# Kernel optimization log

Measured on AMD Instinct MI355X. Metric: run time of the kernel, lower is better.

## Reference

```python
import jax, jax.numpy as jnp
import numpy as np

C1 = 512  # channels1 (query input dim)
C = 512   # channels (model dim)


def setup_inputs() -> dict:
    key = jax.random.key(0)
    ks = jax.random.split(key, 12)
    B, Lq, Lk = 8, 2048, 2048
    s1 = 1.0 / np.sqrt(C1)
    s = 1.0 / np.sqrt(C)
    return {
        "rep": jax.random.normal(ks[0], (B, Lq, C1), dtype=jnp.float32),
        "rep1": jax.random.normal(ks[1], (B, Lk, C), dtype=jnp.float32),
        "Wq_w": jax.random.uniform(ks[2], (C1, C), jnp.float32, -s1, s1),
        "Wq_b": jax.random.uniform(ks[3], (C,), jnp.float32, -s1, s1),
        "Wk_w": jax.random.uniform(ks[4], (C, C), jnp.float32, -s, s),
        "Wk_b": jax.random.uniform(ks[5], (C,), jnp.float32, -s, s),
        "Wv_w": jax.random.uniform(ks[6], (C, C), jnp.float32, -s, s),
        "Wv_b": jax.random.uniform(ks[7], (C,), jnp.float32, -s, s),
        "FC_w": jax.random.uniform(ks[8], (C, C), jnp.float32, -s, s),
        "FC_b": jax.random.uniform(ks[9], (C,), jnp.float32, -s, s),
    }


def reference(rep, rep1, Wq_w, Wq_b, Wk_w, Wk_b, Wv_w, Wv_b, FC_w, FC_b):
    # Linear + ReLU projections (single head)
    q = jax.nn.relu(jnp.einsum('blc,cd->bld', rep, Wq_w) + Wq_b)    # [B,Lq,C]
    k = jax.nn.relu(jnp.einsum('blc,cd->bld', rep1, Wk_w) + Wk_b)   # [B,Lk,C]
    v = jax.nn.relu(jnp.einsum('blc,cd->bld', rep1, Wv_w) + Wv_b)   # [B,Lk,C]
    scores = jnp.einsum('bqd,bkd->bqk', q, k) / jnp.sqrt(jnp.float32(C))
    attn = jax.nn.softmax(scores, axis=-1)                           # [B,Lq,Lk]
    out = jnp.einsum('bqk,bkd->bqd', attn, v)                        # [B,Lq,C]
    out = jax.nn.relu(jnp.einsum('bld,de->ble', out, FC_w) + FC_b)
    return out
```

## Files before the change

### kernel.cpp

```cpp
#include <hip/hip_runtime.h>


typedef __attribute__((ext_vector_type(8))) short short8;
typedef __attribute__((ext_vector_type(4))) float f32x4;

#define SEQ 2048
#define CH 512
#define NB 8
#define MTOT (NB * SEQ)

#define GLDS16(gp, lp)                                                                  \
  __builtin_amdgcn_global_load_lds((const __attribute__((address_space(1))) void*)(gp), \
                                   (__attribute__((address_space(3))) void*)(lp), 16, 0, 0)

__device__ __forceinline__ unsigned short f2bf(float f) {
  unsigned u = __float_as_uint(f);
  u += 0x7fffu + ((u >> 16) & 1u);
  return (unsigned short)(u >> 16);
}

__global__ void cvt_bf16_kernel(const float* __restrict__ in0, unsigned short* __restrict__ out0,
                                const float* __restrict__ in1, unsigned short* __restrict__ out1) {
  int blk = blockIdx.x;
  const float* in = (blk < 4096) ? in0 : in1;
  unsigned short* out = (blk < 4096) ? out0 : out1;
  blk &= 4095;
  long i = ((long)blk * 256 + threadIdx.x) * 8;
  float4 a = *(const float4*)(in + i);
  float4 b = *(const float4*)(in + i + 4);
  ushort4 o0, o1;
  o0.x = f2bf(a.x); o0.y = f2bf(a.y); o0.z = f2bf(a.z); o0.w = f2bf(a.w);
  o1.x = f2bf(b.x); o1.y = f2bf(b.y); o1.z = f2bf(b.z); o1.w = f2bf(b.w);
  *(ushort4*)(out + i) = o0;
  *(ushort4*)(out + i + 4) = o1;
}

__global__ __launch_bounds__(256) void wtrans_kernel(const float* __restrict__ W0,
                                                     const float* __restrict__ W1,
                                                     const float* __restrict__ W2,
                                                     const float* __restrict__ W3,
                                                     unsigned short* __restrict__ Wt) {
  __shared__ __attribute__((aligned(16))) unsigned short tile[64 * 72];
  const int z = blockIdx.z;
  const float* W = (z == 0) ? W0 : (z == 1) ? W1 : (z == 2) ? W2 : W3;
  unsigned short* Wtz = Wt + (long)z * 512 * 512;
  const int t = threadIdx.x;
  const int k0 = blockIdx.y * 64, n0 = blockIdx.x * 64;
  const int r = t >> 4, cq = (t & 15) * 4;
#pragma unroll
  for (int j = 0; j < 4; ++j) {
    int row = r + 16 * j;
    float4 v = *(const float4*)&W[(long)(k0 + row) * 512 + n0 + cq];
    tile[row * 72 + cq + 0] = f2bf(v.x);
    tile[row * 72 + cq + 1] = f2bf(v.y);
    tile[row * 72 + cq + 2] = f2bf(v.z);
    tile[row * 72 + cq + 3] = f2bf(v.w);
  }
  __syncthreads();
#pragma unroll
  for (int j = 0; j < 4; ++j) {
    int row = r + 16 * j;
    ushort4 o;
    o.x = tile[(cq + 0) * 72 + row];
    o.y = tile[(cq + 1) * 72 + row];
    o.z = tile[(cq + 2) * 72 + row];
    o.w = tile[(cq + 3) * 72 + row];
    *(ushort4*)&Wtz[(long)(n0 + row) * 512 + k0 + cq] = o;
  }
}

__global__ __launch_bounds__(256) void vtrans_kernel(const unsigned short* __restrict__ V,
                                                     unsigned short* __restrict__ Vt) {
  __shared__ __attribute__((aligned(16))) unsigned short tile[64 * 72];
  const int t = threadIdx.x;
  const int b = blockIdx.z;
  const int kk0 = blockIdx.y * 64;
  const int d0 = blockIdx.x * 64;
  const unsigned short* Vb = V + (long)b * SEQ * CH;
  unsigned short* Vtb = Vt + (long)b * CH * SEQ;
  const int r = t >> 4, cq = (t & 15) * 4;
#pragma unroll
  for (int j = 0; j < 4; ++j) {
    int row = r + 16 * j;
    ushort4 v = *(const ushort4*)&Vb[(long)(kk0 + row) * CH + d0 + cq];
    tile[row * 72 + cq + 0] = v.x;
    tile[row * 72 + cq + 1] = v.y;
    tile[row * 72 + cq + 2] = v.z;
    tile[row * 72 + cq + 3] = v.w;
  }
  __syncthreads();
#pragma unroll
  for (int j = 0; j < 4; ++j) {
    int row = r + 16 * j;
    ushort4 o;
    o.x = tile[(cq + 0) * 72 + row];
    o.y = tile[(cq + 1) * 72 + row];
    o.z = tile[(cq + 2) * 72 + row];
    o.w = tile[(cq + 3) * 72 + row];
    *(ushort4*)&Vtb[(long)(d0 + row) * SEQ + kk0 + cq] = o;
  }
}

template <int EPI, int LDA, int LDB, int LDO, int K, int BK>
__global__ __launch_bounds__(256) void gemm_nt(const unsigned short* __restrict__ A, long sAb,
                                               const unsigned short* __restrict__ Bt, long sBb,
                                               const float* __restrict__ bias,
                                               float* __restrict__ rowsum, long sRb,
                                               void* __restrict__ outp, long sOb) {
  __shared__ __attribute__((aligned(16))) unsigned short smem[2 * 128 * BK];
  unsigned short* Al = smem;
  unsigned short* Bl = smem + 128 * BK;
  const int t = threadIdx.x;
  const int w = t >> 6, l = t & 63;
  const int wr = w >> 1, wc = w & 1;
  const int lr = l & 15, lg = l >> 4;
  const int bz = blockIdx.z;
  const long m0 = (long)blockIdx.y * 128, n0 = (long)blockIdx.x * 128;
  const int NC = BK / 8;
  const int rl = l / NC, cc0 = l % NC;
  unsigned short* la = &Al[32 * w * BK];
  unsigned short* lb = &Bl[32 * w * BK];
  const unsigned short* gaJ[(BK == 128) ? 4 : 1];
  const unsigned short* gbJ[(BK == 128) ? 4 : 1];
  if (BK == 64) {
    const int srow = 32 * w + rl;
    const int sxor = (cc0 ^ (rl & 7)) * 8;
    gaJ[0] = A + bz * sAb + (long)(m0 + srow) * LDA + sxor;
    gbJ[0] = Bt + bz * sBb + (long)(n0 + srow) * LDB + sxor;
  } else {
#pragma unroll
    for (int jm = 0; jm < 4; ++jm) {
      const int srow = 32 * w + 4 * jm + rl;
      const int sxor = (cc0 ^ ((4 * jm + rl) & 15)) * 8;
      gaJ[jm] = A + bz * sAb + (long)(m0 + srow) * LDA + sxor;
      gbJ[jm] = Bt + bz * sBb + (long)(n0 + srow) * LDB + sxor;
    }
  }

  f32x4 acc[4][4] = {};
  for (int k0 = 0; k0 < K; k0 += BK) {
    if (BK == 64) {
#pragma unroll
      for (int j = 0; j < 4; ++j) {
        GLDS16(gaJ[0] + (long)8 * j * LDA, la + j * 8 * 64);
        GLDS16(gbJ[0] + (long)8 * j * LDB, lb + j * 8 * 64);
      }
      gaJ[0] += BK; gbJ[0] += BK;
    } else {
#pragma unroll
      for (int jm = 0; jm < 4; ++jm) {
        GLDS16(gaJ[jm], la + jm * 4 * 128);
        GLDS16(gaJ[jm] + (long)16 * LDA, la + (16 + 4 * jm) * 128);
        GLDS16(gbJ[jm], lb + jm * 4 * 128);
        GLDS16(gbJ[jm] + (long)16 * LDB, lb + (16 + 4 * jm) * 128);
        gaJ[jm] += BK; gbJ[jm] += BK;
      }
    }
    __syncthreads();
#pragma unroll
    for (int h = 0; h < BK / 32; ++h) {
      short8 af[4], bfr[4];
#pragma unroll
      for (int i = 0; i < 4; ++i) {
        const int kc = ((h * 4 + lg) ^ (lr & (NC - 1))) * 8;
        af[i]  = *(short8*)&Al[(64 * wr + 16 * i + lr) * BK + kc];
        bfr[i] = *(short8*)&Bl[(64 * wc + 16 * i + lr) * BK + kc];
      }
#pragma unroll
      for (int mi = 0; mi < 4; ++mi)
#pragma unroll
        for (int ni = 0; ni < 4; ++ni)
          acc[mi][ni] =
              __builtin_amdgcn_mfma_f32_16x16x32_bf16(af[mi], bfr[ni], acc[mi][ni], 0, 0, 0);
    }
    __syncthreads();
  }

  if (EPI == 1 || EPI == 6 || EPI == 2) {
    unsigned short* patch = smem;
    float bv[4];
    if (EPI == 1) {
#pragma unroll
      for (int ni = 0; ni < 4; ++ni) bv[ni] = bias[n0 + 64 * wc + 16 * ni + lr];
    }
    float rsum[4][4] = {};
#pragma unroll
    for (int mi = 0; mi < 4; ++mi)
#pragma unroll
      for (int ni = 0; ni < 4; ++ni)
#pragma unroll
        for (int r = 0; r < 4; ++r) {
          const int m = 64 * wr + 16 * mi + 4 * lg + r;
          const int n = 64 * wc + 16 * ni + lr;
          float a = acc[mi][ni][r];
          unsigned short ob;
          if (EPI == 1)      ob = f2bf(fmaxf(a + bv[ni], 0.0f));
          else if (EPI == 6) ob = f2bf(a);
          else {
            float p = exp2f(a * 0.06375872f);
            ob = f2bf(p);
            rsum[mi][r] += __uint_as_float((unsigned)ob << 16);
          }
          patch[m * 128 + ((n >> 3) ^ (m & 15)) * 8 + (n & 7)] = ob;
        }
    __syncthreads();
    unsigned short* O = (unsigned short*)outp + bz * sOb;
    const int q = t & 3;
#pragma unroll
    for (int p = 0; p < 2; ++p) {
      const int m = 64 * p + (t >> 2);
#pragma unroll
      for (int i = 0; i < 4; ++i) {
        const int cc = i * 4 + q;
        short8 x = *(short8*)&patch[m * 128 + ((cc ^ (m & 15)) * 8)];
        *(short8*)&O[(m0 + m) * LDO + n0 + cc * 8] = x;
      }
    }
    if (EPI == 2) {
      float* rsw = rowsum + bz * sRb;
#pragma unroll
      for (int off = 1; off < 16; off <<= 1)
#pragma unroll
        for (int mi = 0; mi < 4; ++mi)
#pragma unroll
          for (int r = 0; r < 4; ++r) rsum[mi][r] += __shfl_xor(rsum[mi][r], off);
      if (lr == 0) {
#pragma unroll
        for (int mi = 0; mi < 4; ++mi)
#pragma unroll
          for (int r = 0; r < 4; ++r)
            atomicAdd(&rsw[m0 + 64 * wr + 16 * mi + 4 * lg + r], rsum[mi][r]);
      }
    }
  } else {
    float* patchF = (float*)smem;
    float bv[4];
#pragma unroll
    for (int ni = 0; ni < 4; ++ni) bv[ni] = bias[n0 + 64 * wc + 16 * ni + lr];
    const float* rs = rowsum + bz * sRb;
    float inv[4][4];
#pragma unroll
    for (int mi = 0; mi < 4; ++mi)
#pragma unroll
      for (int r = 0; r < 4; ++r)
        inv[mi][r] = 1.0f / rs[m0 + 64 * wr + 16 * mi + 4 * lg + r];
#pragma unroll
    for (int mi = 0; mi < 4; ++mi)
#pragma unroll
      for (int ni = 0; ni < 4; ++ni)
#pragma unroll
        for (int r = 0; r < 4; ++r) {
          const int m = 64 * wr + 16 * mi + 4 * lg + r;
          const int n = 64 * wc + 16 * ni + lr;
          patchF[m * 128 + ((n >> 2) ^ (m & 31)) * 4 + (n & 3)] =
              fmaxf(acc[mi][ni][r] * inv[mi][r] + bv[ni], 0.0f);
        }
    __syncthreads();
    float* O = (float*)outp + bz * sOb;
    const int q = t & 3;
#pragma unroll
    for (int p = 0; p < 2; ++p) {
      const int m = 64 * p + (t >> 2);
#pragma unroll
      for (int i = 0; i < 8; ++i) {
        const int cc = i * 4 + q;
        f32x4 x = *(f32x4*)&patchF[m * 128 + ((cc ^ (m & 31)) * 4)];
        *(f32x4*)&O[(m0 + m) * LDO + n0 + cc * 4] = x;
      }
    }
  }
}

extern "C" void kernel_launch(void* const* d_in, const int* in_sizes, int n_in,
                              void* d_out, int out_size, void* d_ws, size_t ws_size,
                              hipStream_t stream) {
  const float* rep  = (const float*)d_in[0];
  const float* rep1 = (const float*)d_in[1];
  const float* Wq_w = (const float*)d_in[2];
  const float* Wq_b = (const float*)d_in[3];
  const float* Wk_w = (const float*)d_in[4];
  const float* Wk_b = (const float*)d_in[5];
  const float* Wv_w = (const float*)d_in[6];
  const float* Wv_b = (const float*)d_in[7];
  const float* FC_w = (const float*)d_in[8];
  const float* FC_b = (const float*)d_in[9];
  float* out = (float*)d_out;
  char* ws = (char*)d_ws;

  const size_t MB = 1024 * 1024;
  unsigned short* Qb     = (unsigned short*)(ws + 0 * MB);
  unsigned short* KVb    = (unsigned short*)(ws + 16 * MB);
  unsigned short* repb   = (unsigned short*)(ws + 48 * MB);
  unsigned short* rep1b  = (unsigned short*)(ws + 64 * MB);
  unsigned short* Wt4    = (unsigned short*)(ws + 80 * MB);
  float*          biasKV = (float*)(ws + 82 * MB);
  unsigned short* Pbuf   = (unsigned short*)(ws + 83 * MB);
  float*          rowsum = (float*)(ws + 147 * MB);
  const size_t need = 148 * MB;
  if (ws_size < need) return;

  unsigned short* WtQ = Wt4;
  unsigned short* WtKV = Wt4 + 512 * 512;
  unsigned short* WtF = Wt4 + 3 * 512 * 512;
  unsigned short* VFn = repb;
  unsigned short* VFt = rep1b;

  hipMemsetAsync(rowsum, 0, MTOT * 4, stream);
  hipMemcpyAsync(biasKV, Wk_b, 512 * 4, hipMemcpyDeviceToDevice, stream);
  hipMemcpyAsync(biasKV + 512, Wv_b, 512 * 4, hipMemcpyDeviceToDevice, stream);

  cvt_bf16_kernel<<<8192, 256, 0, stream>>>(rep, repb, rep1, rep1b);
  wtrans_kernel<<<dim3(8, 8, 4), 256, 0, stream>>>(Wq_w, Wk_w, Wv_w, FC_w, Wt4);

  gemm_nt<1, CH, CH, CH, CH, 64><<<dim3(4, 128, 1), 256, 0, stream>>>(
      repb, 0, WtQ, 0, Wq_b, nullptr, 0, Qb, 0);
  gemm_nt<1, CH, CH, 1024, CH, 64><<<dim3(8, 128, 1), 256, 0, stream>>>(
      rep1b, 0, WtKV, 0, biasKV, nullptr, 0, KVb, 0);

  gemm_nt<6, 1024, CH, CH, CH, 64><<<dim3(4, 16, 8), 256, 0, stream>>>(
      KVb + 512, (long)SEQ * 1024, WtF, 0, nullptr, nullptr, 0, VFn, (long)SEQ * CH);

  vtrans_kernel<<<dim3(8, 32, 8), 256, 0, stream>>>(VFn, VFt);

  gemm_nt<2, CH, 1024, SEQ, CH, 64><<<dim3(16, 16, 8), 256, 0, stream>>>(
      Qb, (long)SEQ * CH, KVb, (long)SEQ * 1024, nullptr, rowsum, SEQ,
      Pbuf, (long)SEQ * SEQ);

  gemm_nt<5, SEQ, SEQ, CH, SEQ, 128><<<dim3(4, 16, 8), 256, 0, stream>>>(
      Pbuf, (long)SEQ * SEQ, VFt, (long)CH * SEQ, FC_b, rowsum, SEQ,
      (void*)out, (long)SEQ * CH);
}
```

Before: 326.2 us.

## Merge prep and projection kernels, emit transposed VF directly, drop vtrans

Folds the bf16 conversion, weight transposes, bias copy and rowsum zeroing into one prep kernel, replacing the memset/memcpy calls. Merges the Q and KV projection GEMMs into one launch. Computes the V·FC product transposed by swapping operands, so the separate V transpose kernel goes away. Switches the final P·VF GEMM from BK=128 to BK=64. The aim is fewer launches and less transpose traffic, at the cost of less K-depth per stage in the largest GEMM.

```diff
diff --git a/kernel.cpp b/kernel.cpp
--- a/kernel.cpp
+++ b/kernel.cpp
@@ -19,143 +19,98 @@
   return (unsigned short)(u >> 16);
 }
 
-__global__ void cvt_bf16_kernel(const float* __restrict__ in0, unsigned short* __restrict__ out0,
-                                const float* __restrict__ in1, unsigned short* __restrict__ out1) {
-  int blk = blockIdx.x;
-  const float* in = (blk < 4096) ? in0 : in1;
-  unsigned short* out = (blk < 4096) ? out0 : out1;
-  blk &= 4095;
-  long i = ((long)blk * 256 + threadIdx.x) * 8;
-  float4 a = *(const float4*)(in + i);
-  float4 b = *(const float4*)(in + i + 4);
-  ushort4 o0, o1;
-  o0.x = f2bf(a.x); o0.y = f2bf(a.y); o0.z = f2bf(a.z); o0.w = f2bf(a.w);
-  o1.x = f2bf(b.x); o1.y = f2bf(b.y); o1.z = f2bf(b.z); o1.w = f2bf(b.w);
-  *(ushort4*)(out + i) = o0;
-  *(ushort4*)(out + i + 4) = o1;
-}
-
-__global__ __launch_bounds__(256) void wtrans_kernel(const float* __restrict__ W0,
-                                                     const float* __restrict__ W1,
-                                                     const float* __restrict__ W2,
-                                                     const float* __restrict__ W3,
-                                                     unsigned short* __restrict__ Wt) {
+__global__ __launch_bounds__(256) void prep_kernel(
+    const float* __restrict__ rep, const float* __restrict__ rep1,
+    unsigned short* __restrict__ repb, unsigned short* __restrict__ rep1b,
+    const float* __restrict__ W0, const float* __restrict__ W1,
+    const float* __restrict__ W2, const float* __restrict__ W3,
+    unsigned short* __restrict__ Wt,
+    const float* __restrict__ Wk_b, const float* __restrict__ Wv_b,
+    float* __restrict__ biasKV, float* __restrict__ rowsum) {
   __shared__ __attribute__((aligned(16))) unsigned short tile[64 * 72];
-  const int z = blockIdx.z;
-  const float* W = (z == 0) ? W0 : (z == 1) ? W1 : (z == 2) ? W2 : W3;
-  unsigned short* Wtz = Wt + (long)z * 512 * 512;
+  const int blk = blockIdx.x;
   const int t = threadIdx.x;
-  const int k0 = blockIdx.y * 64, n0 = blockIdx.x * 64;
-  const int r = t >> 4, cq = (t & 15) * 4;
-#pragma unroll
-  for (int j = 0; j < 4; ++j) {
-    int row = r + 16 * j;
-    float4 v = *(const float4*)&W[(long)(k0 + row) * 512 + n0 + cq];
-    tile[row * 72 + cq + 0] = f2bf(v.x);
-    tile[row * 72 + cq + 1] = f2bf(v.y);
-    tile[row * 72 + cq + 2] = f2bf(v.z);
-    tile[row * 72 + cq + 3] = f2bf(v.w);
+  if (blk < 8192) {
+    const float* in = (blk < 4096) ? rep : rep1;
+    unsigned short* out = (blk < 4096) ? repb : rep1b;
+    long i = ((long)(blk & 4095) * 256 + t) * 8;
+    float4 a = *(const float4*)(in + i);
+    float4 b = *(const float4*)(in + i + 4);
+    ushort4 o0, o1;
+    o0.x = f2bf(a.x); o0.y = f2bf(a.y); o0.z = f2bf(a.z); o0.w = f2bf(a.w);
+    o1.x = f2bf(b.x); o1.y = f2bf(b.y); o1.z = f2bf(b.z); o1.w = f2bf(b.w);
+    *(ushort4*)(out + i) = o0;
+    *(ushort4*)(out + i + 4) = o1;
+  } else if (blk < 8448) {
+    const int zz = blk - 8192;
+    const int z = zz >> 6;
+    const int bx = zz & 7, by = (zz >> 3) & 7;
+    const float* W = (z == 0) ? W0 : (z == 1) ? W1 : (z == 2) ? W2 : W3;
+    unsigned short* Wtz = Wt + (long)z * 512 * 512;
+    const int k0 = by * 64, n0 = bx * 64;
+    const int r = t >> 4, cq = (t & 15) * 4;
+#pragma unroll
+    for (int j = 0; j < 4; ++j) {
+      int row = r + 16 * j;
+      float4 v = *(const float4*)&W[(long)(k0 + row) * 512 + n0 + cq];
+      tile[row * 72 + cq + 0] = f2bf(v.x);
+      tile[row * 72 + cq + 1] = f2bf(v.y);
+      tile[row * 72 + cq + 2] = f2bf(v.z);
+      tile[row * 72 + cq + 3] = f2bf(v.w);
+    }
+    __syncthreads();
+#pragma unroll
+    for (int j = 0; j < 4; ++j) {
+      int row = r + 16 * j;
+      ushort4 o;
+      o.x = tile[(cq + 0) * 72 + row];
+      o.y = tile[(cq + 1) * 72 + row];
+      o.z = tile[(cq + 2) * 72 + row];
+      o.w = tile[(cq + 3) * 72 + row];
+      *(ushort4*)&Wtz[(long)(n0 + row) * 512 + k0 + cq] = o;
+    }
+  } else if (blk == 8448) {
+    biasKV[t] = Wk_b[t];
+    biasKV[t + 256] = Wk_b[t + 256];
+    biasKV[t + 512] = Wv_b[t];
+    biasKV[t + 768] = Wv_b[t + 256];
+  } else {
+    const int zb = blk - 8449;
+    f32x4 z4 = {0.f, 0.f, 0.f, 0.f};
+    *(f32x4*)&rowsum[(zb * 256 + t) * 4] = z4;
   }
-  __syncthreads();
-#pragma unroll
-  for (int j = 0; j < 4; ++j) {
-    int row = r + 16 * j;
-    ushort4 o;
-    o.x = tile[(cq + 0) * 72 + row];
-    o.y = tile[(cq + 1) * 72 + row];
-    o.z = tile[(cq + 2) * 72 + row];
-    o.w = tile[(cq + 3) * 72 + row];
-    *(ushort4*)&Wtz[(long)(n0 + row) * 512 + k0 + cq] = o;
-  }
-}
-
-__global__ __launch_bounds__(256) void vtrans_kernel(const unsigned short* __restrict__ V,
-                                                     unsigned short* __restrict__ Vt) {
-  __shared__ __attribute__((aligned(16))) unsigned short tile[64 * 72];
-  const int t = threadIdx.x;
-  const int b = blockIdx.z;
-  const int kk0 = blockIdx.y * 64;
-  const int d0 = blockIdx.x * 64;
-  const unsigned short* Vb = V + (long)b * SEQ * CH;
-  unsigned short* Vtb = Vt + (long)b * CH * SEQ;
-  const int r = t >> 4, cq = (t & 15) * 4;
-#pragma unroll
-  for (int j = 0; j < 4; ++j) {
-    int row = r + 16 * j;
-    ushort4 v = *(const ushort4*)&Vb[(long)(kk0 + row) * CH + d0 + cq];
-    tile[row * 72 + cq + 0] = v.x;
-    tile[row * 72 + cq + 1] = v.y;
-    tile[row * 72 + cq + 2] = v.z;
-    tile[row * 72 + cq + 3] = v.w;
-  }
-  __syncthreads();
-#pragma unroll
-  for (int j = 0; j < 4; ++j) {
-    int row = r + 16 * j;
-    ushort4 o;
-    o.x = tile[(cq + 0) * 72 + row];
-    o.y = tile[(cq + 1) * 72 + row];
-    o.z = tile[(cq + 2) * 72 + row];
-    o.w = tile[(cq + 3) * 72 + row];
-    *(ushort4*)&Vtb[(long)(d0 + row) * SEQ + kk0 + cq] = o;
-  }
 }
 
 template <int EPI, int LDA, int LDB, int LDO, int K, int BK>
-__global__ __launch_bounds__(256) void gemm_nt(const unsigned short* __restrict__ A, long sAb,
-                                               const unsigned short* __restrict__ Bt, long sBb,
-                                               const float* __restrict__ bias,
-                                               float* __restrict__ rowsum, long sRb,
-                                               void* __restrict__ outp, long sOb) {
-  __shared__ __attribute__((aligned(16))) unsigned short smem[2 * 128 * BK];
+__device__ __forceinline__ void gemm_body(const unsigned short* __restrict__ A,
+                                          const unsigned short* __restrict__ Bt,
+                                          const float* __restrict__ bias,
+                                          float* __restrict__ rowsum,
+                                          void* __restrict__ outp,
+                                          long m0, long n0, unsigned short* smem) {
   unsigned short* Al = smem;
   unsigned short* Bl = smem + 128 * BK;
   const int t = threadIdx.x;
   const int w = t >> 6, l = t & 63;
   const int wr = w >> 1, wc = w & 1;
   const int lr = l & 15, lg = l >> 4;
-  const int bz = blockIdx.z;
-  const long m0 = (long)blockIdx.y * 128, n0 = (long)blockIdx.x * 128;
-  const int NC = BK / 8;
+  constexpr int NC = BK / 8;
   const int rl = l / NC, cc0 = l % NC;
   unsigned short* la = &Al[32 * w * BK];
   unsigned short* lb = &Bl[32 * w * BK];
-  const unsigned short* gaJ[(BK == 128) ? 4 : 1];
-  const unsigned short* gbJ[(BK == 128) ? 4 : 1];
-  if (BK == 64) {
-    const int srow = 32 * w + rl;
-    const int sxor = (cc0 ^ (rl & 7)) * 8;
-    gaJ[0] = A + bz * sAb + (long)(m0 + srow) * LDA + sxor;
-    gbJ[0] = Bt + bz * sBb + (long)(n0 + srow) * LDB + sxor;
-  } else {
-#pragma unroll
-    for (int jm = 0; jm < 4; ++jm) {
-      const int srow = 32 * w + 4 * jm + rl;
-      const int sxor = (cc0 ^ ((4 * jm + rl) & 15)) * 8;
-      gaJ[jm] = A + bz * sAb + (long)(m0 + srow) * LDA + sxor;
-      gbJ[jm] = Bt + bz * sBb + (long)(n0 + srow) * LDB + sxor;
-    }
-  }
+  const int srow = 32 * w + rl;
+  const int sxor = (cc0 ^ (rl & (NC - 1))) * 8;
+  const unsigned short* ga = A + (m0 + srow) * (long)LDA + sxor;
+  const unsigned short* gb = Bt + (n0 + srow) * (long)LDB + sxor;
 
   f32x4 acc[4][4] = {};
   for (int k0 = 0; k0 < K; k0 += BK) {
-    if (BK == 64) {
-#pragma unroll
-      for (int j = 0; j < 4; ++j) {
-        GLDS16(gaJ[0] + (long)8 * j * LDA, la + j * 8 * 64);
-        GLDS16(gbJ[0] + (long)8 * j * LDB, lb + j * 8 * 64);
-      }
-      gaJ[0] += BK; gbJ[0] += BK;
-    } else {
-#pragma unroll
-      for (int jm = 0; jm < 4; ++jm) {
-        GLDS16(gaJ[jm], la + jm * 4 * 128);
-        GLDS16(gaJ[jm] + (long)16 * LDA, la + (16 + 4 * jm) * 128);
-        GLDS16(gbJ[jm], lb + jm * 4 * 128);
-        GLDS16(gbJ[jm] + (long)16 * LDB, lb + (16 + 4 * jm) * 128);
-        gaJ[jm] += BK; gbJ[jm] += BK;
-      }
-    }
+#pragma unroll
+    for (int j = 0; j < 4; ++j) {
+      GLDS16(ga + (long)8 * j * LDA, la + j * 8 * BK);
+      GLDS16(gb + (long)8 * j * LDB, lb + j * 8 * BK);
+    }
+    ga += BK; gb += BK;
     __syncthreads();
 #pragma unroll
     for (int h = 0; h < BK / 32; ++h) {
@@ -204,7 +159,7 @@
           patch[m * 128 + ((n >> 3) ^ (m & 15)) * 8 + (n & 7)] = ob;
         }
     __syncthreads();
-    unsigned short* O = (unsigned short*)outp + bz * sOb;
+    unsigned short* O = (unsigned short*)outp;
     const int q = t & 3;
 #pragma unroll
     for (int p = 0; p < 2; ++p) {
@@ -217,7 +172,6 @@
       }
     }
     if (EPI == 2) {
-      float* rsw = rowsum + bz * sRb;
 #pragma unroll
       for (int off = 1; off < 16; off <<= 1)
 #pragma unroll
@@ -229,7 +183,7 @@
         for (int mi = 0; mi < 4; ++mi)
 #pragma unroll
           for (int r = 0; r < 4; ++r)
-            atomicAdd(&rsw[m0 + 64 * wr + 16 * mi + 4 * lg + r], rsum[mi][r]);
+            atomicAdd(&rowsum[m0 + 64 * wr + 16 * mi + 4 * lg + r], rsum[mi][r]);
       }
     }
   } else {
@@ -237,13 +191,12 @@
     float bv[4];
 #pragma unroll
     for (int ni = 0; ni < 4; ++ni) bv[ni] = bias[n0 + 64 * wc + 16 * ni + lr];
-    const float* rs = rowsum + bz * sRb;
     float inv[4][4];
 #pragma unroll
     for (int mi = 0; mi < 4; ++mi)
 #pragma unroll
       for (int r = 0; r < 4; ++r)
-        inv[mi][r] = 1.0f / rs[m0 + 64 * wr + 16 * mi + 4 * lg + r];
+        inv[mi][r] = 1.0f / rowsum[m0 + 64 * wr + 16 * mi + 4 * lg + r];
 #pragma unroll
     for (int mi = 0; mi < 4; ++mi)
 #pragma unroll
@@ -256,7 +209,7 @@
               fmaxf(acc[mi][ni][r] * inv[mi][r] + bv[ni], 0.0f);
         }
     __syncthreads();
-    float* O = (float*)outp + bz * sOb;
+    float* O = (float*)outp;
     const int q = t & 3;
 #pragma unroll
     for (int p = 0; p < 2; ++p) {
@@ -268,6 +221,40 @@
         *(f32x4*)&O[(m0 + m) * LDO + n0 + cc * 4] = x;
       }
     }
+  }
+}
+
+template <int EPI, int LDA, int LDB, int LDO, int K, int BK>
+__global__ __launch_bounds__(256) void gemm_nt(const unsigned short* __restrict__ A, long sAb,
+                                               const unsigned short* __restrict__ Bt, long sBb,
+                                               const float* __restrict__ bias,
+                                               float* __restrict__ rowsum, long sRb,
+                                               void* __restrict__ outp, long sOb) {
+  constexpr int SM = (EPI == 5) ? 32768 : 2 * 128 * BK;
+  __shared__ __attribute__((aligned(16))) unsigned short smem[SM];
+  const int bz = blockIdx.z;
+  void* o = (EPI == 5) ? (void*)((float*)outp + (long)bz * sOb)
+                       : (void*)((unsigned short*)outp + (long)bz * sOb);
+  float* rs = rowsum ? rowsum + (long)bz * sRb : nullptr;
+  gemm_body<EPI, LDA, LDB, LDO, K, BK>(A + (long)bz * sAb, Bt + (long)bz * sBb, bias, rs, o,
+                                       (long)blockIdx.y * 128, (long)blockIdx.x * 128, smem);
+}
+
+__global__ __launch_bounds__(256) void proj_kernel(const unsigned short* __restrict__ repb,
+                                                   const unsigned short* __restrict__ rep1b,
+                                                   const unsigned short* __restrict__ Wt,
+                                                   const float* __restrict__ Wq_b,
+                                                   const float* __restrict__ biasKV,
+                                                   unsigned short* __restrict__ Qb,
+                                                   unsigned short* __restrict__ KVb) {
+  __shared__ __attribute__((aligned(16))) unsigned short smem[2 * 128 * 64];
+  const long m0 = (long)blockIdx.y * 128;
+  if (blockIdx.x < 4) {
+    gemm_body<1, CH, CH, CH, CH, 64>(repb, Wt, Wq_b, nullptr, Qb, m0,
+                                     (long)blockIdx.x * 128, smem);
+  } else {
+    gemm_body<1, CH, CH, 1024, CH, 64>(rep1b, Wt + 512 * 512, biasKV, nullptr, KVb, m0,
+                                       (long)(blockIdx.x - 4) * 128, smem);
   }
 }
 
@@ -300,33 +287,22 @@
   if (ws_size < need) return;
 
   unsigned short* WtQ = Wt4;
-  unsigned short* WtKV = Wt4 + 512 * 512;
   unsigned short* WtF = Wt4 + 3 * 512 * 512;
-  unsigned short* VFn = repb;
-  unsigned short* VFt = rep1b;
-
-  hipMemsetAsync(rowsum, 0, MTOT * 4, stream);
-  hipMemcpyAsync(biasKV, Wk_b, 512 * 4, hipMemcpyDeviceToDevice, stream);
-  hipMemcpyAsync(biasKV + 512, Wv_b, 512 * 4, hipMemcpyDeviceToDevice, stream);
-
-  cvt_bf16_kernel<<<8192, 256, 0, stream>>>(rep, repb, rep1, rep1b);
-  wtrans_kernel<<<dim3(8, 8, 4), 256, 0, stream>>>(Wq_w, Wk_w, Wv_w, FC_w, Wt4);
-
-  gemm_nt<1, CH, CH, CH, CH, 64><<<dim3(4, 128, 1), 256, 0, stream>>>(
-      repb, 0, WtQ, 0, Wq_b, nullptr, 0, Qb, 0);
-  gemm_nt<1, CH, CH, 1024, CH, 64><<<dim3(8, 128, 1), 256, 0, stream>>>(
-      rep1b, 0, WtKV, 0, biasKV, nullptr, 0, KVb, 0);
-
-  gemm_nt<6, 1024, CH, CH, CH, 64><<<dim3(4, 16, 8), 256, 0, stream>>>(
-      KVb + 512, (long)SEQ * 1024, WtF, 0, nullptr, nullptr, 0, VFn, (long)SEQ * CH);
-
-  vtrans_kernel<<<dim3(8, 32, 8), 256, 0, stream>>>(VFn, VFt);
+  unsigned short* VFt = repb;
+
+  prep_kernel<<<8465, 256, 0, stream>>>(rep, rep1, repb, rep1b, Wq_w, Wk_w, Wv_w, FC_w,
+                                        Wt4, Wk_b, Wv_b, biasKV, rowsum);
+
+  proj_kernel<<<dim3(12, 128), 256, 0, stream>>>(repb, rep1b, Wt4, Wq_b, biasKV, Qb, KVb);
+
+  gemm_nt<6, CH, 1024, SEQ, CH, 64><<<dim3(16, 4, 8), 256, 0, stream>>>(
+      WtF, 0, KVb + 512, (long)SEQ * 1024, nullptr, nullptr, 0, VFt, (long)CH * SEQ);
 
   gemm_nt<2, CH, 1024, SEQ, CH, 64><<<dim3(16, 16, 8), 256, 0, stream>>>(
       Qb, (long)SEQ * CH, KVb, (long)SEQ * 1024, nullptr, rowsum, SEQ,
       Pbuf, (long)SEQ * SEQ);
 
-  gemm_nt<5, SEQ, SEQ, CH, SEQ, 128><<<dim3(4, 16, 8), 256, 0, stream>>>(
+  gemm_nt<5, SEQ, SEQ, CH, SEQ, 64><<<dim3(4, 16, 8), 256, 0, stream>>>(
       Pbuf, (long)SEQ * SEQ, VFt, (long)CH * SEQ, FC_b, rowsum, SEQ,
       (void*)out, (long)SEQ * CH);
 }
```

Result: faster. 296.7 us (-9.0%).
